# Kernel tuning notes

Hardware: AMD Instinct MI355X
Metric: run time of the kernel (lower is better)

The kernel has to match this reference:

```python
import jax, jax.numpy as jnp
import numpy as np

# DeepSeek-V3 MoE config (matches init_kwargs)
H = 1024          # hidden_size
I = 704           # moe_intermediate_size
E = 64            # n_routed_experts
TOP_K = 8         # num_experts_per_tok
NG = 8            # n_group
TOPK_GROUP = 4    # topk_group
N_SHARED = 2      # n_shared_experts
ROUTED_SCALE = 2.5
S_I = I * N_SHARED  # shared expert intermediate size


def setup_inputs() -> dict:
    key = jax.random.key(0)
    ks = jax.random.split(key, 10)
    sc = 0.02
    return {
        "hidden_states": jax.random.normal(ks[0], (1, 1024, H), dtype=jnp.float32),
        "gate_w": sc * jax.random.normal(ks[1], (E, H), dtype=jnp.float32),
        "gate_bias": sc * jax.random.normal(ks[2], (E,), dtype=jnp.float32),  # e_score_correction_bias
        "Wg": sc * jax.random.normal(ks[3], (E, I, H), dtype=jnp.float32),
        "Wu": sc * jax.random.normal(ks[4], (E, I, H), dtype=jnp.float32),
        "Wd": sc * jax.random.normal(ks[5], (E, H, I), dtype=jnp.float32),
        "Sg": sc * jax.random.normal(ks[6], (S_I, H), dtype=jnp.float32),
        "Su": sc * jax.random.normal(ks[7], (S_I, H), dtype=jnp.float32),
        "Sd": sc * jax.random.normal(ks[8], (H, S_I), dtype=jnp.float32),
    }


def _route(x, gate_w, gate_bias):
    # x: [T, H] -> dense routing weight matrix [T, E]
    T = x.shape[0]
    logits = x @ gate_w.T                         # [T, E] (fp32, as HF casts to float32)
    scores = jax.nn.sigmoid(logits)
    scores_for_choice = scores + gate_bias[None, :]
    # group scores: sum of top-2 expert scores in each group
    grp = scores_for_choice.reshape(T, NG, E // NG)
    group_scores = jnp.sum(jax.lax.top_k(grp, 2)[0], axis=-1)      # [T, NG]
    _, gidx = jax.lax.top_k(group_scores, TOPK_GROUP)              # [T, TOPK_GROUP]
    gmask = jnp.zeros((T, NG), dtype=scores.dtype).at[
        jnp.arange(T)[:, None], gidx].set(1.0)                      # [T, NG]
    emask = jnp.repeat(gmask, E // NG, axis=1)                      # [T, E]
    masked = jnp.where(emask > 0, scores_for_choice, 0.0)
    _, topk_idx = jax.lax.top_k(masked, TOP_K)                      # [T, TOP_K]
    topk_w = jnp.take_along_axis(scores, topk_idx, axis=1)          # gather from UNbiased scores
    topk_w = topk_w / (jnp.sum(topk_w, axis=-1, keepdims=True) + 1e-20)  # norm_topk_prob
    topk_w = topk_w * ROUTED_SCALE
    # dense [T, E] combine weights (zeros for unrouted experts)
    rw = jnp.zeros((T, E), dtype=scores.dtype).at[
        jnp.arange(T)[:, None], topk_idx].add(topk_w)
    return rw


def _mlp(x, gw, uw, dw):
    # SwiGLU MLP: down(silu(gate(x)) * up(x)), no biases
    return (jax.nn.silu(x @ gw.T) * (x @ uw.T)) @ dw.T


def reference(hidden_states, gate_w, gate_bias, Wg, Wu, Wd, Sg, Su, Sd):
    B, S, _ = hidden_states.shape
    x = hidden_states.reshape(B * S, H)                 # [T, H]
    rw = _route(x, gate_w, gate_bias)                   # [T, E]
    # dense reference: run every expert on every token, weighted combine
    expert_out = jax.vmap(lambda gw_, uw_, dw_: _mlp(x, gw_, uw_, dw_))(Wg, Wu, Wd)  # [E, T, H]
    routed = jnp.einsum('eth,te->th', expert_out, rw)   # [T, H]
    shared = _mlp(x, Sg, Su, Sd)                        # [T, H]
    out = (routed + shared).reshape(B, S, H)
    return out
```

## Files before the change

kernel.cpp:

```cpp
#include <hip/hip_runtime.h>
#include <hip/hip_bf16.h>
#include <cstdint>
#include <cstddef>

#define T_TOK 1024
#define H_DIM 1024
#define I_DIM 704
#define E_NUM 64
#define TOPK 8
#define NGRP 8
#define GSIZE 8
#define TOPKG 4
#define SI_DIM 1408
#define RSCALE 2.5f
#define NSLOT (T_TOK * TOPK)

#define AP 72

typedef short bf16x8 __attribute__((ext_vector_type(8)));
typedef float f32x4 __attribute__((ext_vector_type(4)));

__device__ inline unsigned pk2(float x, float y) {
    __hip_bfloat162 h2 = __float22bfloat162_rn(make_float2(x, y));
    unsigned u; __builtin_memcpy(&u, &h2, 4); return u;
}
__device__ inline unsigned short bf1(float x) {
    __hip_bfloat16 h = __float2bfloat16(x);
    unsigned short u; __builtin_memcpy(&u, &h, 2); return u;
}

__global__ __launch_bounds__(64) void route_kernel(
    const float* __restrict__ x, const float* __restrict__ gw, const float* __restrict__ gb,
    int* __restrict__ counts, int* __restrict__ tk_idx, float* __restrict__ tk_w)
{
    const int t = blockIdx.x;
    __shared__ float xs[H_DIM];
    __shared__ float raw[E_NUM];
    __shared__ float sc[E_NUM];
    __shared__ float masked[E_NUM];
    __shared__ float gsc[NGRP];
    const int tid = threadIdx.x;

    const float4* xrow = (const float4*)(x + (size_t)t * H_DIM);
    for (int i = tid; i < H_DIM / 4; i += 64) ((float4*)xs)[i] = xrow[i];
    __syncthreads();

    float a = 0.f;
    const float* w = gw + (size_t)tid * H_DIM;
    for (int h = 0; h < H_DIM; h += 4) {
        float4 w4 = *(const float4*)(w + h);
        a += xs[h] * w4.x + xs[h+1] * w4.y + xs[h+2] * w4.z + xs[h+3] * w4.w;
    }
    float s = 1.f / (1.f + expf(-a));
    raw[tid] = s;
    sc[tid] = s + gb[tid];
    __syncthreads();

    if (tid == 0) {
        for (int g = 0; g < NGRP; ++g) {
            float m1 = -1e30f, m2 = -1e30f;
            for (int j = 0; j < GSIZE; ++j) {
                float v = sc[g * GSIZE + j];
                if (v > m1) { m2 = m1; m1 = v; }
                else if (v > m2) { m2 = v; }
            }
            gsc[g] = m1 + m2;
        }
        bool gsel[NGRP];
        for (int g = 0; g < NGRP; ++g) gsel[g] = false;
        for (int k = 0; k < TOPKG; ++k) {
            int best = -1; float bv = -1e30f;
            for (int g = 0; g < NGRP; ++g)
                if (!gsel[g] && gsc[g] > bv) { bv = gsc[g]; best = g; }
            gsel[best] = true;
        }
        for (int e = 0; e < E_NUM; ++e)
            masked[e] = gsel[e / GSIZE] ? sc[e] : 0.0f;
        int idx[TOPK];
        float wsum = 0.f;
        for (int k = 0; k < TOPK; ++k) {
            int best = 0; float bv = -1e30f;
            for (int e = 0; e < E_NUM; ++e)
                if (masked[e] > bv) { bv = masked[e]; best = e; }
            masked[best] = -1e30f;
            idx[k] = best;
            wsum += raw[best];
        }
        float inv = RSCALE / (wsum + 1e-20f);
        for (int k = 0; k < TOPK; ++k) {
            tk_idx[t * TOPK + k] = idx[k];
            tk_w[t * TOPK + k] = raw[idx[k]] * inv;
            atomicAdd(&counts[idx[k]], 1);
        }
    }
}

__global__ void zero_kernel(int* counts, int* fillc)
{
    int i = threadIdx.x;
    if (i < E_NUM) { counts[i] = 0; fillc[i] = 0; }
}

__global__ void scan_kernel(const int* __restrict__ counts, int* __restrict__ offs)
{
    if (threadIdx.x == 0) {
        int acc = 0;
        for (int e = 0; e < E_NUM; ++e) { offs[e] = acc; acc += counts[e]; }
    }
}

__global__ void fill_kernel(const int* __restrict__ tk_idx, const float* __restrict__ tk_w,
                            const int* __restrict__ offs, int* __restrict__ fillc,
                            int* __restrict__ tok_list, float* __restrict__ w_list)
{
    int t = blockIdx.x * blockDim.x + threadIdx.x;
    if (t >= T_TOK) return;
    for (int k = 0; k < TOPK; ++k) {
        int e = tk_idx[t * TOPK + k];
        int pos = offs[e] + atomicAdd(&fillc[e], 1);
        tok_list[pos] = t;
        w_list[pos] = tk_w[t * TOPK + k];
    }
}

__global__ __launch_bounds__(256) void gateup_routed_mfma(
    const float* __restrict__ x, const float* __restrict__ Wg, const float* __restrict__ Wu,
    const int* __restrict__ offs, const int* __restrict__ counts,
    const int* __restrict__ tok_list, const float* __restrict__ w_list,
    unsigned short* __restrict__ act)
{
    const int e = blockIdx.z;
    const int cnt = counts[e];
    const int m0 = blockIdx.y * 128;
    if (m0 >= cnt) return;
    const int off = offs[e];
    const int n0 = blockIdx.x * 64;

    __shared__ unsigned short As[128 * AP];
    __shared__ unsigned short Bg[64 * AP];
    __shared__ unsigned short Bu[64 * AP];
    __shared__ int toks[128];
    __shared__ float wts[128];

    const int tid = threadIdx.x;
    if (tid < 128) {
        int s = m0 + tid;
        toks[tid] = (s < cnt) ? tok_list[off + s] : -1;
        wts[tid]  = (s < cnt) ? w_list[off + s] : 0.f;
    }
    __syncthreads();

    const int lane = tid & 63;
    const int wv = tid >> 6;
    const int lr = lane & 15;
    const int lq = lane >> 4;

    f32x4 accg[2][4], accu[2][4];
    #pragma unroll
    for (int i = 0; i < 2; ++i)
        #pragma unroll
        for (int j = 0; j < 4; ++j) {
            accg[i][j] = (f32x4){0.f, 0.f, 0.f, 0.f};
            accu[i][j] = (f32x4){0.f, 0.f, 0.f, 0.f};
        }

    const float* wgp = Wg + (size_t)e * I_DIM * H_DIM + (size_t)n0 * H_DIM;
    const float* wup = Wu + (size_t)e * I_DIM * H_DIM + (size_t)n0 * H_DIM;

    const int ar = tid >> 4;
    const int ac = (tid & 15) * 4;

    for (int k0 = 0; k0 < H_DIM; k0 += 64) {
        #pragma unroll
        for (int p = 0; p < 8; ++p) {
            int r = ar + p * 16;
            int tkn = toks[r];
            float4 v = make_float4(0.f, 0.f, 0.f, 0.f);
            if (tkn >= 0) v = *(const float4*)(x + (size_t)tkn * H_DIM + k0 + ac);
            *(uint2*)&As[r * AP + ac] = make_uint2(pk2(v.x, v.y), pk2(v.z, v.w));
        }
        #pragma unroll
        for (int p = 0; p < 4; ++p) {
            int r = ar + p * 16;
            float4 g = *(const float4*)(wgp + (size_t)r * H_DIM + k0 + ac);
            *(uint2*)&Bg[r * AP + ac] = make_uint2(pk2(g.x, g.y), pk2(g.z, g.w));
            float4 u = *(const float4*)(wup + (size_t)r * H_DIM + k0 + ac);
            *(uint2*)&Bu[r * AP + ac] = make_uint2(pk2(u.x, u.y), pk2(u.z, u.w));
        }
        __syncthreads();
        #pragma unroll
        for (int ks = 0; ks < 2; ++ks) {
            bf16x8 a0 = *(const bf16x8*)&As[(wv * 32 + lr) * AP + ks * 32 + lq * 8];
            bf16x8 a1 = *(const bf16x8*)&As[(wv * 32 + 16 + lr) * AP + ks * 32 + lq * 8];
            #pragma unroll
            for (int nj = 0; nj < 4; ++nj) {
                bf16x8 bg = *(const bf16x8*)&Bg[(nj * 16 + lr) * AP + ks * 32 + lq * 8];
                bf16x8 bu = *(const bf16x8*)&Bu[(nj * 16 + lr) * AP + ks * 32 + lq * 8];
                accg[0][nj] = __builtin_amdgcn_mfma_f32_16x16x32_bf16(a0, bg, accg[0][nj], 0, 0, 0);
                accg[1][nj] = __builtin_amdgcn_mfma_f32_16x16x32_bf16(a1, bg, accg[1][nj], 0, 0, 0);
                accu[0][nj] = __builtin_amdgcn_mfma_f32_16x16x32_bf16(a0, bu, accu[0][nj], 0, 0, 0);
                accu[1][nj] = __builtin_amdgcn_mfma_f32_16x16x32_bf16(a1, bu, accu[1][nj], 0, 0, 0);
            }
        }
        __syncthreads();
    }

    #pragma unroll
    for (int mi = 0; mi < 2; ++mi) {
        #pragma unroll
        for (int r = 0; r < 4; ++r) {
            int srow = wv * 32 + mi * 16 + lq * 4 + r;
            if (m0 + srow < cnt) {
                float w = wts[srow];
                unsigned short* ap = act + (size_t)(off + m0 + srow) * I_DIM + n0 + lr;
                #pragma unroll
                for (int nj = 0; nj < 4; ++nj) {
                    float g = accg[mi][nj][r];
                    float u = accu[mi][nj][r];
                    float a = w * (g / (1.f + __expf(-g))) * u;
                    ap[nj * 16] = bf1(a);
                }
            }
        }
    }
}

__global__ __launch_bounds__(256) void down_routed_mfma(
    const unsigned short* __restrict__ act, const float* __restrict__ Wd,
    const int* __restrict__ offs, const int* __restrict__ counts,
    const int* __restrict__ tok_list, float* __restrict__ out)
{
    const int e = blockIdx.z;
    const int cnt = counts[e];
    const int m0 = blockIdx.y * 128;
    if (m0 >= cnt) return;
    const int off = offs[e];
    const int n0 = blockIdx.x * 64;

    __shared__ unsigned short As[128 * AP];
    __shared__ unsigned short Bs[64 * AP];
    __shared__ int toks[128];

    const int tid = threadIdx.x;
    if (tid < 128) {
        int s = m0 + tid;
        toks[tid] = (s < cnt) ? tok_list[off + s] : 0;
    }
    __syncthreads();

    const int lane = tid & 63;
    const int wv = tid >> 6;
    const int lr = lane & 15;
    const int lq = lane >> 4;

    f32x4 acc[2][4];
    #pragma unroll
    for (int i = 0; i < 2; ++i)
        #pragma unroll
        for (int j = 0; j < 4; ++j)
            acc[i][j] = (f32x4){0.f, 0.f, 0.f, 0.f};

    const float* wdp = Wd + (size_t)e * H_DIM * I_DIM + (size_t)n0 * I_DIM;
    const unsigned short* ap0 = act + (size_t)(off + m0) * I_DIM;
    const int ar = tid >> 4;
    const int ac = (tid & 15) * 4;

    for (int k0 = 0; k0 < I_DIM; k0 += 64) {
        #pragma unroll
        for (int p = 0; p < 8; ++p) {
            int r = ar + p * 16;
            uint2 v = make_uint2(0u, 0u);
            if (m0 + r < cnt) v = *(const uint2*)(ap0 + (size_t)r * I_DIM + k0 + ac);
            *(uint2*)&As[r * AP + ac] = v;
        }
        #pragma unroll
        for (int p = 0; p < 4; ++p) {
            int r = ar + p * 16;
            float4 w4 = *(const float4*)(wdp + (size_t)r * I_DIM + k0 + ac);
            *(uint2*)&Bs[r * AP + ac] = make_uint2(pk2(w4.x, w4.y), pk2(w4.z, w4.w));
        }
        __syncthreads();
        #pragma unroll
        for (int ks = 0; ks < 2; ++ks) {
            bf16x8 a0 = *(const bf16x8*)&As[(wv * 32 + lr) * AP + ks * 32 + lq * 8];
            bf16x8 a1 = *(const bf16x8*)&As[(wv * 32 + 16 + lr) * AP + ks * 32 + lq * 8];
            #pragma unroll
            for (int nj = 0; nj < 4; ++nj) {
                bf16x8 b = *(const bf16x8*)&Bs[(nj * 16 + lr) * AP + ks * 32 + lq * 8];
                acc[0][nj] = __builtin_amdgcn_mfma_f32_16x16x32_bf16(a0, b, acc[0][nj], 0, 0, 0);
                acc[1][nj] = __builtin_amdgcn_mfma_f32_16x16x32_bf16(a1, b, acc[1][nj], 0, 0, 0);
            }
        }
        __syncthreads();
    }

    #pragma unroll
    for (int mi = 0; mi < 2; ++mi) {
        #pragma unroll
        for (int r = 0; r < 4; ++r) {
            int srow = wv * 32 + mi * 16 + lq * 4 + r;
            if (m0 + srow < cnt) {
                int t = toks[srow];
                float* op = out + (size_t)t * H_DIM + n0 + lr;
                #pragma unroll
                for (int nj = 0; nj < 4; ++nj)
                    atomicAdd(&op[nj * 16], acc[mi][nj][r]);
            }
        }
    }
}

__global__ __launch_bounds__(256) void gateup_shared_mfma(
    const float* __restrict__ x, const float* __restrict__ Sg, const float* __restrict__ Su,
    unsigned short* __restrict__ sact)
{
    const int m0 = blockIdx.y * 128;
    const int n0 = blockIdx.x * 64;

    __shared__ unsigned short As[128 * AP];
    __shared__ unsigned short Bg[64 * AP];
    __shared__ unsigned short Bu[64 * AP];

    const int tid = threadIdx.x;
    const int lane = tid & 63;
    const int wv = tid >> 6;
    const int lr = lane & 15;
    const int lq = lane >> 4;

    f32x4 accg[2][4], accu[2][4];
    #pragma unroll
    for (int i = 0; i < 2; ++i)
        #pragma unroll
        for (int j = 0; j < 4; ++j) {
            accg[i][j] = (f32x4){0.f, 0.f, 0.f, 0.f};
            accu[i][j] = (f32x4){0.f, 0.f, 0.f, 0.f};
        }

    const float* gp = Sg + (size_t)n0 * H_DIM;
    const float* up = Su + (size_t)n0 * H_DIM;
    const int ar = tid >> 4;
    const int ac = (tid & 15) * 4;

    for (int k0 = 0; k0 < H_DIM; k0 += 64) {
        #pragma unroll
        for (int p = 0; p < 8; ++p) {
            int r = ar + p * 16;
            float4 v = *(const float4*)(x + (size_t)(m0 + r) * H_DIM + k0 + ac);
            *(uint2*)&As[r * AP + ac] = make_uint2(pk2(v.x, v.y), pk2(v.z, v.w));
        }
        #pragma unroll
        for (int p = 0; p < 4; ++p) {
            int r = ar + p * 16;
            float4 g = *(const float4*)(gp + (size_t)r * H_DIM + k0 + ac);
            *(uint2*)&Bg[r * AP + ac] = make_uint2(pk2(g.x, g.y), pk2(g.z, g.w));
            float4 u = *(const float4*)(up + (size_t)r * H_DIM + k0 + ac);
            *(uint2*)&Bu[r * AP + ac] = make_uint2(pk2(u.x, u.y), pk2(u.z, u.w));
        }
        __syncthreads();
        #pragma unroll
        for (int ks = 0; ks < 2; ++ks) {
            bf16x8 a0 = *(const bf16x8*)&As[(wv * 32 + lr) * AP + ks * 32 + lq * 8];
            bf16x8 a1 = *(const bf16x8*)&As[(wv * 32 + 16 + lr) * AP + ks * 32 + lq * 8];
            #pragma unroll
            for (int nj = 0; nj < 4; ++nj) {
                bf16x8 bg = *(const bf16x8*)&Bg[(nj * 16 + lr) * AP + ks * 32 + lq * 8];
                bf16x8 bu = *(const bf16x8*)&Bu[(nj * 16 + lr) * AP + ks * 32 + lq * 8];
                accg[0][nj] = __builtin_amdgcn_mfma_f32_16x16x32_bf16(a0, bg, accg[0][nj], 0, 0, 0);
                accg[1][nj] = __builtin_amdgcn_mfma_f32_16x16x32_bf16(a1, bg, accg[1][nj], 0, 0, 0);
                accu[0][nj] = __builtin_amdgcn_mfma_f32_16x16x32_bf16(a0, bu, accu[0][nj], 0, 0, 0);
                accu[1][nj] = __builtin_amdgcn_mfma_f32_16x16x32_bf16(a1, bu, accu[1][nj], 0, 0, 0);
            }
        }
        __syncthreads();
    }

    #pragma unroll
    for (int mi = 0; mi < 2; ++mi) {
        #pragma unroll
        for (int r = 0; r < 4; ++r) {
            int trow = m0 + wv * 32 + mi * 16 + lq * 4 + r;
            unsigned short* sp = sact + (size_t)trow * SI_DIM + n0 + lr;
            #pragma unroll
            for (int nj = 0; nj < 4; ++nj) {
                float g = accg[mi][nj][r];
                float u = accu[mi][nj][r];
                float a = (g / (1.f + __expf(-g))) * u;
                sp[nj * 16] = bf1(a);
            }
        }
    }
}

__global__ __launch_bounds__(256) void down_shared_mfma(
    const unsigned short* __restrict__ sact, const float* __restrict__ Sd,
    float* __restrict__ out)
{
    const int m0 = blockIdx.y * 128;
    const int n0 = blockIdx.x * 64;

    __shared__ unsigned short As[128 * AP];
    __shared__ unsigned short Bs[64 * AP];

    const int tid = threadIdx.x;
    const int lane = tid & 63;
    const int wv = tid >> 6;
    const int lr = lane & 15;
    const int lq = lane >> 4;

    f32x4 acc[2][4];
    #pragma unroll
    for (int i = 0; i < 2; ++i)
        #pragma unroll
        for (int j = 0; j < 4; ++j)
            acc[i][j] = (f32x4){0.f, 0.f, 0.f, 0.f};

    const float* wp = Sd + (size_t)n0 * SI_DIM;
    const int ar = tid >> 4;
    const int ac = (tid & 15) * 4;

    for (int k0 = 0; k0 < SI_DIM; k0 += 64) {
        #pragma unroll
        for (int p = 0; p < 8; ++p) {
            int r = ar + p * 16;
            uint2 v = *(const uint2*)(sact + (size_t)(m0 + r) * SI_DIM + k0 + ac);
            *(uint2*)&As[r * AP + ac] = v;
        }
        #pragma unroll
        for (int p = 0; p < 4; ++p) {
            int r = ar + p * 16;
            float4 w4 = *(const float4*)(wp + (size_t)r * SI_DIM + k0 + ac);
            *(uint2*)&Bs[r * AP + ac] = make_uint2(pk2(w4.x, w4.y), pk2(w4.z, w4.w));
        }
        __syncthreads();
        #pragma unroll
        for (int ks = 0; ks < 2; ++ks) {
            bf16x8 a0 = *(const bf16x8*)&As[(wv * 32 + lr) * AP + ks * 32 + lq * 8];
            bf16x8 a1 = *(const bf16x8*)&As[(wv * 32 + 16 + lr) * AP + ks * 32 + lq * 8];
            #pragma unroll
            for (int nj = 0; nj < 4; ++nj) {
                bf16x8 b = *(const bf16x8*)&Bs[(nj * 16 + lr) * AP + ks * 32 + lq * 8];
                acc[0][nj] = __builtin_amdgcn_mfma_f32_16x16x32_bf16(a0, b, acc[0][nj], 0, 0, 0);
                acc[1][nj] = __builtin_amdgcn_mfma_f32_16x16x32_bf16(a1, b, acc[1][nj], 0, 0, 0);
            }
        }
        __syncthreads();
    }

    #pragma unroll
    for (int mi = 0; mi < 2; ++mi) {
        #pragma unroll
        for (int r = 0; r < 4; ++r) {
            int trow = m0 + wv * 32 + mi * 16 + lq * 4 + r;
            float* op = out + (size_t)trow * H_DIM + n0 + lr;
            #pragma unroll
            for (int nj = 0; nj < 4; ++nj)
                op[nj * 16] = acc[mi][nj][r];
        }
    }
}

extern "C" void kernel_launch(void* const* d_in, const int* in_sizes, int n_in,
                              void* d_out, int out_size, void* d_ws, size_t ws_size,
                              hipStream_t stream)
{
    const float* x  = (const float*)d_in[0];
    const float* gw = (const float*)d_in[1];
    const float* gb = (const float*)d_in[2];
    const float* Wg = (const float*)d_in[3];
    const float* Wu = (const float*)d_in[4];
    const float* Wd = (const float*)d_in[5];
    const float* Sg = (const float*)d_in[6];
    const float* Su = (const float*)d_in[7];
    const float* Sd = (const float*)d_in[8];
    float* out = (float*)d_out;

    unsigned short* act  = (unsigned short*)d_ws;
    unsigned short* sact = act + (size_t)NSLOT * I_DIM;
    int* counts   = (int*)(sact + (size_t)T_TOK * SI_DIM);
    int* fillc    = counts + 64;
    int* offs     = fillc + 64;
    int* tk_idx   = offs + 64;
    float* tk_w   = (float*)(tk_idx + NSLOT);
    int* tok_list = (int*)(tk_w + NSLOT);
    float* w_list = (float*)(tok_list + NSLOT);

    zero_kernel<<<1, 64, 0, stream>>>(counts, fillc);
    route_kernel<<<T_TOK, 64, 0, stream>>>(x, gw, gb, counts, tk_idx, tk_w);
    scan_kernel<<<1, 64, 0, stream>>>(counts, offs);
    fill_kernel<<<4, 256, 0, stream>>>(tk_idx, tk_w, offs, fillc, tok_list, w_list);

    gateup_routed_mfma<<<dim3(11, 8, 64), 256, 0, stream>>>(x, Wg, Wu, offs, counts, tok_list, w_list, act);
    gateup_shared_mfma<<<dim3(22, 8, 1), 256, 0, stream>>>(x, Sg, Su, sact);
    down_shared_mfma<<<dim3(16, 8, 1), 256, 0, stream>>>(sact, Sd, out);
    down_routed_mfma<<<dim3(16, 8, 64), 256, 0, stream>>>(act, Wd, offs, counts, tok_list, out);
}
```

Before: 843.7 us.

## Compact routed GEMM grids via block list and replace atomics with slot combine

The scan kernel now builds a compact list of (expert, row-offset) tiles, so the routed gate/up and down GEMMs launch up to 128 row-blocks instead of 8x64, most of which exited immediately. The down kernel writes per-slot outputs to a new workspace buffer instead of doing float atomicAdd into the token output. A new combine kernel then sums each token's eight slot rows into the output. This removes empty block launches and atomic contention, at the cost of an extra 32MB intermediate buffer write and read plus an extra launch. MAXBLK=128 assumes the total tile count never exceeds 128 (64 experts plus ceil spillover), which holds when counts sum to 8192.

```diff
diff --git a/kernel.cpp b/kernel.cpp
--- a/kernel.cpp
+++ b/kernel.cpp
@@ -14,6 +14,7 @@
 #define SI_DIM 1408
 #define RSCALE 2.5f
 #define NSLOT (T_TOK * TOPK)
+#define MAXBLK 128
 
 #define AP 72
 
@@ -101,17 +102,24 @@
     if (i < E_NUM) { counts[i] = 0; fillc[i] = 0; }
 }
 
-__global__ void scan_kernel(const int* __restrict__ counts, int* __restrict__ offs)
+__global__ void scan_kernel(const int* __restrict__ counts, int* __restrict__ offs,
+                            int* __restrict__ blk_e, int* __restrict__ blk_s0,
+                            int* __restrict__ nblk)
 {
     if (threadIdx.x == 0) {
         int acc = 0;
         for (int e = 0; e < E_NUM; ++e) { offs[e] = acc; acc += counts[e]; }
+        int n = 0;
+        for (int e = 0; e < E_NUM; ++e)
+            for (int t = 0; t < counts[e]; t += 128) { blk_e[n] = e; blk_s0[n] = t; ++n; }
+        nblk[0] = n;
     }
 }
 
 __global__ void fill_kernel(const int* __restrict__ tk_idx, const float* __restrict__ tk_w,
                             const int* __restrict__ offs, int* __restrict__ fillc,
-                            int* __restrict__ tok_list, float* __restrict__ w_list)
+                            int* __restrict__ tok_list, float* __restrict__ w_list,
+                            int* __restrict__ tk_pos)
 {
     int t = blockIdx.x * blockDim.x + threadIdx.x;
     if (t >= T_TOK) return;
@@ -120,6 +128,7 @@
         int pos = offs[e] + atomicAdd(&fillc[e], 1);
         tok_list[pos] = t;
         w_list[pos] = tk_w[t * TOPK + k];
+        tk_pos[t * TOPK + k] = pos;
     }
 }
 
@@ -127,12 +136,14 @@
     const float* __restrict__ x, const float* __restrict__ Wg, const float* __restrict__ Wu,
     const int* __restrict__ offs, const int* __restrict__ counts,
     const int* __restrict__ tok_list, const float* __restrict__ w_list,
+    const int* __restrict__ blk_e, const int* __restrict__ blk_s0, const int* __restrict__ nblk,
     unsigned short* __restrict__ act)
 {
-    const int e = blockIdx.z;
+    const int by = blockIdx.y;
+    if (by >= nblk[0]) return;
+    const int e = blk_e[by];
+    const int m0 = blk_s0[by];
     const int cnt = counts[e];
-    const int m0 = blockIdx.y * 128;
-    if (m0 >= cnt) return;
     const int off = offs[e];
     const int n0 = blockIdx.x * 64;
 
@@ -228,26 +239,21 @@
 __global__ __launch_bounds__(256) void down_routed_mfma(
     const unsigned short* __restrict__ act, const float* __restrict__ Wd,
     const int* __restrict__ offs, const int* __restrict__ counts,
-    const int* __restrict__ tok_list, float* __restrict__ out)
-{
-    const int e = blockIdx.z;
+    const int* __restrict__ blk_e, const int* __restrict__ blk_s0, const int* __restrict__ nblk,
+    float* __restrict__ slot_out)
+{
+    const int by = blockIdx.y;
+    if (by >= nblk[0]) return;
+    const int e = blk_e[by];
+    const int m0 = blk_s0[by];
     const int cnt = counts[e];
-    const int m0 = blockIdx.y * 128;
-    if (m0 >= cnt) return;
     const int off = offs[e];
     const int n0 = blockIdx.x * 64;
 
     __shared__ unsigned short As[128 * AP];
     __shared__ unsigned short Bs[64 * AP];
-    __shared__ int toks[128];
 
     const int tid = threadIdx.x;
-    if (tid < 128) {
-        int s = m0 + tid;
-        toks[tid] = (s < cnt) ? tok_list[off + s] : 0;
-    }
-    __syncthreads();
-
     const int lane = tid & 63;
     const int wv = tid >> 6;
     const int lr = lane & 15;
@@ -300,14 +306,31 @@
         for (int r = 0; r < 4; ++r) {
             int srow = wv * 32 + mi * 16 + lq * 4 + r;
             if (m0 + srow < cnt) {
-                int t = toks[srow];
-                float* op = out + (size_t)t * H_DIM + n0 + lr;
+                float* op = slot_out + (size_t)(off + m0 + srow) * H_DIM + n0 + lr;
                 #pragma unroll
                 for (int nj = 0; nj < 4; ++nj)
-                    atomicAdd(&op[nj * 16], acc[mi][nj][r]);
-            }
-        }
-    }
+                    op[nj * 16] = acc[mi][nj][r];
+            }
+        }
+    }
+}
+
+__global__ __launch_bounds__(256) void combine_kernel(
+    const float* __restrict__ slot_out, const int* __restrict__ tk_pos,
+    float* __restrict__ out)
+{
+    const int t = blockIdx.x;
+    __shared__ int pos[TOPK];
+    if (threadIdx.x < TOPK) pos[threadIdx.x] = tk_pos[t * TOPK + threadIdx.x];
+    __syncthreads();
+    const int i = threadIdx.x;
+    float4 a = ((const float4*)(out + (size_t)t * H_DIM))[i];
+    #pragma unroll
+    for (int k = 0; k < TOPK; ++k) {
+        float4 v = ((const float4*)(slot_out + (size_t)pos[k] * H_DIM))[i];
+        a.x += v.x; a.y += v.y; a.z += v.z; a.w += v.w;
+    }
+    ((float4*)(out + (size_t)t * H_DIM))[i] = a;
 }
 
 __global__ __launch_bounds__(256) void gateup_shared_mfma(
@@ -474,7 +497,8 @@
     const float* Sd = (const float*)d_in[8];
     float* out = (float*)d_out;
 
-    unsigned short* act  = (unsigned short*)d_ws;
+    float* slot_out = (float*)d_ws;
+    unsigned short* act  = (unsigned short*)(slot_out + (size_t)NSLOT * H_DIM);
     unsigned short* sact = act + (size_t)NSLOT * I_DIM;
     int* counts   = (int*)(sact + (size_t)T_TOK * SI_DIM);
     int* fillc    = counts + 64;
@@ -483,14 +507,21 @@
     float* tk_w   = (float*)(tk_idx + NSLOT);
     int* tok_list = (int*)(tk_w + NSLOT);
     float* w_list = (float*)(tok_list + NSLOT);
+    int* tk_pos   = (int*)(w_list + NSLOT);
+    int* blk_e    = tk_pos + NSLOT;
+    int* blk_s0   = blk_e + MAXBLK;
+    int* nblk     = blk_s0 + MAXBLK;
 
     zero_kernel<<<1, 64, 0, stream>>>(counts, fillc);
     route_kernel<<<T_TOK, 64, 0, stream>>>(x, gw, gb, counts, tk_idx, tk_w);
-    scan_kernel<<<1, 64, 0, stream>>>(counts, offs);
-    fill_kernel<<<4, 256, 0, stream>>>(tk_idx, tk_w, offs, fillc, tok_list, w_list);
-
-    gateup_routed_mfma<<<dim3(11, 8, 64), 256, 0, stream>>>(x, Wg, Wu, offs, counts, tok_list, w_list, act);
-    gateup_shared_mfma<<<dim3(22, 8, 1), 256, 0, stream>>>(x, Sg, Su, sact);
-    down_shared_mfma<<<dim3(16, 8, 1), 256, 0, stream>>>(sact, Sd, out);
-    down_routed_mfma<<<dim3(16, 8, 64), 256, 0, stream>>>(act, Wd, offs, counts, tok_list, out);
-}
+    scan_kernel<<<1, 64, 0, stream>>>(counts, offs, blk_e, blk_s0, nblk);
+    fill_kernel<<<4, 256, 0, stream>>>(tk_idx, tk_w, offs, fillc, tok_list, w_list, tk_pos);
+
+    gateup_routed_mfma<<<dim3(11, MAXBLK), 256, 0, stream>>>(
+        x, Wg, Wu, offs, counts, tok_list, w_list, blk_e, blk_s0, nblk, act);
+    gateup_shared_mfma<<<dim3(22, 8), 256, 0, stream>>>(x, Sg, Su, sact);
+    down_shared_mfma<<<dim3(16, 8), 256, 0, stream>>>(sact, Sd, out);
+    down_routed_mfma<<<dim3(16, MAXBLK), 256, 0, stream>>>(
+        act, Wd, offs, counts, blk_e, blk_s0, nblk, slot_out);
+    combine_kernel<<<T_TOK, 256, 0, stream>>>(slot_out, tk_pos, out);
+}
```

Measured after the change: 808.2 us. 1.04x faster.
